# Performance work log

Measured on AMD Instinct MI355X. Metric: run time of the kernel, lower is better.

## Reference

```python
import jax, jax.numpy as jnp
import numpy as np

N_NODES = 50000
N_EDGES = 800000
N_FEAT = 256
HIDDEN = 64
N_CLASSES = 16
T_END = 3.0  # opt['time']; rk4 takes one step over [0, 3]


def spline_conv(x, src, dst, p, W, R, b, n):
    """SplineConv, dim=1, kernel_size=2, degree=1 open B-spline, aggr='mean'.
    x: [n, Cin]; src/dst: [E]; p: [E,1] pseudo-coords in [0,1];
    W: [2, Cin, Cout]; R: [Cin, Cout]; b: [Cout]."""
    xj = x[src]  # gather source node features [E, Cin]
    # basis weights for K=2, degree=1: (1-p) on kernel 0, p on kernel 1
    msg = ((1.0 - p) * xj) @ W[0] + (p * xj) @ W[1]  # [E, Cout]
    agg = jax.ops.segment_sum(msg, dst, num_segments=n)
    deg = jax.ops.segment_sum(jnp.ones((msg.shape[0], 1), msg.dtype), dst, num_segments=n)
    return agg / jnp.maximum(deg, 1.0) + x @ R + b


def setup_inputs() -> dict:
    key = jax.random.key(0)
    ks = jax.random.split(key, 20)
    x = jax.random.normal(ks[0], (N_NODES, N_FEAT), jnp.float32)
    edge_attr = jax.random.uniform(ks[1], (N_EDGES, 1), jnp.float32)
    src = jax.random.randint(ks[2], (N_EDGES,), 0, N_NODES)
    dst = jax.random.randint(ks[3], (N_EDGES,), 0, N_NODES)

    def w(k, shape, fan_in):
        s = 1.0 / np.sqrt(fan_in)
        return jax.random.uniform(k, shape, jnp.float32, -s, s)

    # conv1: num_features -> hidden
    W1 = w(ks[4], (2, N_FEAT, HIDDEN), N_FEAT)
    R1 = w(ks[5], (N_FEAT, HIDDEN), N_FEAT)
    b1 = jnp.zeros((HIDDEN,), jnp.float32)
    # ODE func: two stacked SplineConvs hidden -> hidden
    Wa = w(ks[6], (2, HIDDEN, HIDDEN), HIDDEN)
    Ra = w(ks[7], (HIDDEN, HIDDEN), HIDDEN)
    ba = jnp.zeros((HIDDEN,), jnp.float32)
    Wb = w(ks[8], (2, HIDDEN, HIDDEN), HIDDEN)
    Rb = w(ks[9], (HIDDEN, HIDDEN), HIDDEN)
    bb = jnp.zeros((HIDDEN,), jnp.float32)
    # conv2: hidden -> num_classes
    W2 = w(ks[10], (2, HIDDEN, N_CLASSES), HIDDEN)
    R2 = w(ks[11], (HIDDEN, N_CLASSES), HIDDEN)
    b2 = jnp.zeros((N_CLASSES,), jnp.float32)

    return dict(x=x, edge_attr=edge_attr, src=src, dst=dst,
                W1=W1, R1=R1, b1=b1, Wa=Wa, Ra=Ra, ba=ba,
                Wb=Wb, Rb=Rb, bb=bb, W2=W2, R2=R2, b2=b2)


def reference(x, edge_attr, src, dst, W1, R1, b1, Wa, Ra, ba, Wb, Rb, bb, W2, R2, b2):
    n = x.shape[0]
    p = edge_attr
    h = jnp.tanh(spline_conv(x, src, dst, p, W1, R1, b1, n))
    # dropout is identity in eval mode

    def f(y):  # GCNLayer: two stacked SplineConvs, no activation
        y = spline_conv(y, src, dst, p, Wa, Ra, ba, n)
        return spline_conv(y, src, dst, p, Wb, Rb, bb, n)

    # single RK4 step from t=0 to t=T_END (torchdiffeq fixed-grid rk4 on s_span=[0,3])
    k1 = f(h)
    k2 = f(h + 0.5 * T_END * k1)
    k3 = f(h + 0.5 * T_END * k2)
    k4 = f(h + T_END * k3)
    h = h + (T_END / 6.0) * (k1 + 2.0 * k2 + 2.0 * k3 + k4)

    out = jnp.tanh(spline_conv(h, src, dst, p, W2, R2, b2, n))
    return jax.nn.log_softmax(out, axis=1)
```

## Files before the change

### kernel.cpp

```cpp
#include <hip/hip_runtime.h>
#include <math.h>

static inline int ceil_div(int a, int b) { return (a + b - 1) / b; }


__global__ __launch_bounds__(256) void hist_kernel(const int* __restrict__ dst,
                                                   int* __restrict__ deg, int E) {
    int e = blockIdx.x * 256 + threadIdx.x;
    if (e < E) atomicAdd(&deg[dst[e]], 1);
}

__global__ __launch_bounds__(256) void scan_blocksum(const int* __restrict__ deg,
                                                     int* __restrict__ bsum, int n) {
    __shared__ int red[256];
    int t = threadIdx.x;
    int base = blockIdx.x * 2048 + t * 8;
    int s = 0;
    #pragma unroll
    for (int i = 0; i < 8; ++i) {
        int idx = base + i;
        if (idx < n) s += deg[idx];
    }
    red[t] = s;
    __syncthreads();
    #pragma unroll
    for (int off = 128; off >= 1; off >>= 1) {
        if (t < off) red[t] += red[t + off];
        __syncthreads();
    }
    if (t == 0) bsum[blockIdx.x] = red[0];
}

__global__ __launch_bounds__(256) void scan_tops(int* __restrict__ bsum, int nb) {
    __shared__ int sh[256];
    int t = threadIdx.x;
    int orig = (t < nb) ? bsum[t] : 0;
    sh[t] = orig;
    __syncthreads();
    for (int off = 1; off < 256; off <<= 1) {
        int add = (t >= off) ? sh[t - off] : 0;
        __syncthreads();
        sh[t] += add;
        __syncthreads();
    }
    if (t < nb) bsum[t] = sh[t] - orig;
}

__global__ __launch_bounds__(256) void scan_final(const int* __restrict__ deg,
                                                  const int* __restrict__ bsum,
                                                  int* __restrict__ rowp,
                                                  float* __restrict__ invd,
                                                  int n, int E) {
    __shared__ int sh[256];
    int t = threadIdx.x;
    int base = blockIdx.x * 2048 + t * 8;
    int loc[8];
    int s = 0;
    #pragma unroll
    for (int i = 0; i < 8; ++i) {
        int idx = base + i;
        int d = (idx < n) ? deg[idx] : 0;
        loc[i] = d;
        s += d;
    }
    sh[t] = s;
    __syncthreads();
    for (int off = 1; off < 256; off <<= 1) {
        int add = (t >= off) ? sh[t - off] : 0;
        __syncthreads();
        sh[t] += add;
        __syncthreads();
    }
    int run = bsum[blockIdx.x] + (sh[t] - s);
    #pragma unroll
    for (int i = 0; i < 8; ++i) {
        int idx = base + i;
        if (idx < n) {
            rowp[idx] = run;
            int d = loc[i];
            run += d;
            invd[idx] = 1.0f / (float)(d > 1 ? d : 1);
        }
    }
    if (blockIdx.x == 0 && t == 0) rowp[n] = E;
}

__global__ __launch_bounds__(256) void scatter_idx(const int* __restrict__ dst,
                                                   const int* __restrict__ rowp,
                                                   int* __restrict__ fill,
                                                   int* __restrict__ ei, int E) {
    int e = blockIdx.x * 256 + threadIdx.x;
    if (e >= E) return;
    int d = dst[e];
    int pos = rowp[d] + atomicAdd(&fill[d], 1);
    ei[pos] = e;
}

__global__ __launch_bounds__(256) void sort_fill(const int* __restrict__ rowp,
                                                 int* __restrict__ ei,
                                                 const int* __restrict__ src,
                                                 const float* __restrict__ p,
                                                 int* __restrict__ es,
                                                 float* __restrict__ ep, int n) {
    int node = blockIdx.x * 256 + threadIdx.x;
    if (node >= n) return;
    int b = rowp[node], e = rowp[node + 1];
    for (int i = b + 1; i < e; ++i) {
        int key = ei[i];
        int j = i - 1;
        while (j >= b && ei[j] > key) { ei[j + 1] = ei[j]; --j; }
        ei[j + 1] = key;
    }
    for (int i = b; i < e; ++i) {
        int id = ei[i];
        es[i] = src[id];
        ep[i] = p[id];
    }
}

__global__ __launch_bounds__(256) void pack_cat3(const float* __restrict__ W,
                                                 const float* __restrict__ R,
                                                 float* __restrict__ out, int K, int C) {
    int idx = blockIdx.x * 256 + threadIdx.x;
    int M = 3 * C;
    if (idx >= K * M) return;
    int k = idx / M, c = idx % M;
    float v;
    if (c < C)            v = W[k * C + c];
    else if (c < 2 * C)   v = W[K * C + k * C + (c - C)];
    else                  v = R[k * C + (c - 2 * C)];
    out[idx] = v;
}


__global__ __launch_bounds__(256) void edge_agg64_v4(const float* __restrict__ x,
                                                     const int* __restrict__ rowp,
                                                     const int* __restrict__ es,
                                                     const float* __restrict__ ep,
                                                     const float* __restrict__ invd,
                                                     float* __restrict__ agg, int n) {
    int gid = blockIdx.x * 256 + threadIdx.x;
    int node = gid >> 4;
    if (node >= n) return;
    int c4 = (gid & 15) << 2;
    int e = rowp[node], eend = rowp[node + 1];
    float sx = 0.f, sy = 0.f, sz = 0.f, sw = 0.f;
    float px = 0.f, py = 0.f, pz = 0.f, pw = 0.f;
    for (; e + 4 <= eend; e += 4) {
        int s0 = es[e], s1 = es[e + 1], s2 = es[e + 2], s3 = es[e + 3];
        float p0 = ep[e], p1 = ep[e + 1], p2 = ep[e + 2], p3 = ep[e + 3];
        float4 v0 = *reinterpret_cast<const float4*>(&x[(size_t)s0 * 64 + c4]);
        float4 v1 = *reinterpret_cast<const float4*>(&x[(size_t)s1 * 64 + c4]);
        float4 v2 = *reinterpret_cast<const float4*>(&x[(size_t)s2 * 64 + c4]);
        float4 v3 = *reinterpret_cast<const float4*>(&x[(size_t)s3 * 64 + c4]);
        sx += (v0.x + v1.x) + (v2.x + v3.x);
        sy += (v0.y + v1.y) + (v2.y + v3.y);
        sz += (v0.z + v1.z) + (v2.z + v3.z);
        sw += (v0.w + v1.w) + (v2.w + v3.w);
        px = fmaf(p0, v0.x, fmaf(p1, v1.x, fmaf(p2, v2.x, fmaf(p3, v3.x, px))));
        py = fmaf(p0, v0.y, fmaf(p1, v1.y, fmaf(p2, v2.y, fmaf(p3, v3.y, py))));
        pz = fmaf(p0, v0.z, fmaf(p1, v1.z, fmaf(p2, v2.z, fmaf(p3, v3.z, pz))));
        pw = fmaf(p0, v0.w, fmaf(p1, v1.w, fmaf(p2, v2.w, fmaf(p3, v3.w, pw))));
    }
    for (; e < eend; ++e) {
        int s = es[e];
        float pe = ep[e];
        float4 v = *reinterpret_cast<const float4*>(&x[(size_t)s * 64 + c4]);
        sx += v.x; sy += v.y; sz += v.z; sw += v.w;
        px = fmaf(pe, v.x, px); py = fmaf(pe, v.y, py);
        pz = fmaf(pe, v.z, pz); pw = fmaf(pe, v.w, pw);
    }
    float w = invd[node];
    float4 a0 = make_float4((sx - px) * w, (sy - py) * w, (sz - pz) * w, (sw - pw) * w);
    float4 a1 = make_float4(px * w, py * w, pz * w, pw * w);
    *reinterpret_cast<float4*>(&agg[(size_t)node * 128 + c4]) = a0;
    *reinterpret_cast<float4*>(&agg[(size_t)node * 128 + 64 + c4]) = a1;
}

__global__ __launch_bounds__(256) void edge_tf64_v4(const float* __restrict__ yz,
                                                    const int* __restrict__ rowp,
                                                    const int* __restrict__ es,
                                                    const float* __restrict__ ep,
                                                    const float* __restrict__ invd,
                                                    const float* __restrict__ base,
                                                    float* __restrict__ out, int n) {
    int gid = blockIdx.x * 256 + threadIdx.x;
    int node = gid >> 4;
    if (node >= n) return;
    int c4 = (gid & 15) << 2;
    int e = rowp[node], eend = rowp[node + 1];
    float ax = 0.f, ay = 0.f, az = 0.f, aw = 0.f;
    for (; e + 2 <= eend; e += 2) {
        int s0 = es[e], s1 = es[e + 1];
        float p0 = ep[e], p1 = ep[e + 1];
        float4 y0 = *reinterpret_cast<const float4*>(&yz[(size_t)s0 * 128 + c4]);
        float4 z0 = *reinterpret_cast<const float4*>(&yz[(size_t)s0 * 128 + 64 + c4]);
        float4 y1 = *reinterpret_cast<const float4*>(&yz[(size_t)s1 * 128 + c4]);
        float4 z1 = *reinterpret_cast<const float4*>(&yz[(size_t)s1 * 128 + 64 + c4]);
        ax += fmaf(p0, z0.x - y0.x, y0.x) + fmaf(p1, z1.x - y1.x, y1.x);
        ay += fmaf(p0, z0.y - y0.y, y0.y) + fmaf(p1, z1.y - y1.y, y1.y);
        az += fmaf(p0, z0.z - y0.z, y0.z) + fmaf(p1, z1.z - y1.z, y1.z);
        aw += fmaf(p0, z0.w - y0.w, y0.w) + fmaf(p1, z1.w - y1.w, y1.w);
    }
    for (; e < eend; ++e) {
        int s = es[e];
        float pe = ep[e];
        float4 y = *reinterpret_cast<const float4*>(&yz[(size_t)s * 128 + c4]);
        float4 z = *reinterpret_cast<const float4*>(&yz[(size_t)s * 128 + 64 + c4]);
        ax += fmaf(pe, z.x - y.x, y.x);
        ay += fmaf(pe, z.y - y.y, y.y);
        az += fmaf(pe, z.z - y.z, y.z);
        aw += fmaf(pe, z.w - y.w, y.w);
    }
    float w = invd[node];
    size_t idx = (size_t)node * 64 + c4;
    float4 b = *reinterpret_cast<const float4*>(&base[idx]);
    float4 o = make_float4(tanhf(fmaf(ax, w, b.x)), tanhf(fmaf(ay, w, b.y)),
                           tanhf(fmaf(az, w, b.z)), tanhf(fmaf(aw, w, b.w)));
    *reinterpret_cast<float4*>(&out[idx]) = o;
}

__global__ __launch_bounds__(256) void edge_tf16_lsm(const float* __restrict__ yz,
                                                     const int* __restrict__ rowp,
                                                     const int* __restrict__ es,
                                                     const float* __restrict__ ep,
                                                     const float* __restrict__ invd,
                                                     const float* __restrict__ base,
                                                     float* __restrict__ out, int n) {
    int gid = blockIdx.x * 256 + threadIdx.x;
    int node = gid >> 4;
    if (node >= n) return;
    int c = gid & 15;
    int e = rowp[node], eend = rowp[node + 1];
    float a = 0.f;
    for (; e + 4 <= eend; e += 4) {
        int s0 = es[e], s1 = es[e + 1], s2 = es[e + 2], s3 = es[e + 3];
        float p0 = ep[e], p1 = ep[e + 1], p2 = ep[e + 2], p3 = ep[e + 3];
        float y0 = yz[(size_t)s0 * 32 + c],      z0 = yz[(size_t)s0 * 32 + 16 + c];
        float y1 = yz[(size_t)s1 * 32 + c],      z1 = yz[(size_t)s1 * 32 + 16 + c];
        float y2 = yz[(size_t)s2 * 32 + c],      z2 = yz[(size_t)s2 * 32 + 16 + c];
        float y3 = yz[(size_t)s3 * 32 + c],      z3 = yz[(size_t)s3 * 32 + 16 + c];
        a += fmaf(p0, z0 - y0, y0);
        a += fmaf(p1, z1 - y1, y1);
        a += fmaf(p2, z2 - y2, y2);
        a += fmaf(p3, z3 - y3, y3);
    }
    for (; e < eend; ++e) {
        int s = es[e]; float pe = ep[e];
        float y = yz[(size_t)s * 32 + c], z = yz[(size_t)s * 32 + 16 + c];
        a += fmaf(pe, z - y, y);
    }
    float o = tanhf(a * invd[node] + base[(size_t)node * 16 + c]);
    float m = o;
    #pragma unroll
    for (int off = 8; off >= 1; off >>= 1) m = fmaxf(m, __shfl_xor(m, off, 16));
    float ex = expf(o - m);
    float s = ex;
    #pragma unroll
    for (int off = 8; off >= 1; off >>= 1) s += __shfl_xor(s, off, 16);
    out[(size_t)node * 16 + c] = (o - m) - logf(s);
}

__global__ __launch_bounds__(256) void gemm_tiled(
    const float* __restrict__ A0, int lda0, int K0,
    const float* __restrict__ A1, int lda1,
    const float* __restrict__ B,
    int n, int K, int M,
    float* __restrict__ out0, int w0, const float* __restrict__ bias0,
    float* __restrict__ out1, int w1, const float* __restrict__ bias1,
    int split, int mode,
    const float* __restrict__ hbuf, const float* __restrict__ acc_in,
    float* __restrict__ acc_out, float* __restrict__ t_out,
    float c1, float c2, float c3) {
    __shared__ __align__(16) float As[16][68];
    __shared__ __align__(16) float Bs[16][68];
    const int t = threadIdx.x;
    const int row0 = blockIdx.x * 64;
    const int col0 = blockIdx.y * 64;
    const int ty = t >> 4, tx = t & 15;
    const int lrow = t >> 2, lk = (t & 3) << 2;
    const int bkk = t >> 4, bcol = (t & 15) << 2;
    float acc[4][4];
    #pragma unroll
    for (int i = 0; i < 4; ++i)
        #pragma unroll
        for (int j = 0; j < 4; ++j) acc[i][j] = 0.f;

    for (int k0 = 0; k0 < K; k0 += 16) {
        float4 av = make_float4(0.f, 0.f, 0.f, 0.f);
        {
            int r = row0 + lrow;
            if (r < n) {
                int kk = k0 + lk;
                const float* src = (kk < K0)
                    ? (A0 + (size_t)r * lda0 + kk)
                    : (A1 + (size_t)r * lda1 + (kk - K0));
                av = *reinterpret_cast<const float4*>(src);
            }
        }
        float4 bv = make_float4(0.f, 0.f, 0.f, 0.f);
        {
            int c = col0 + bcol;
            int kk = k0 + bkk;
            if (c < M) bv = *reinterpret_cast<const float4*>(B + (size_t)kk * M + c);
        }
        As[lk + 0][lrow] = av.x; As[lk + 1][lrow] = av.y;
        As[lk + 2][lrow] = av.z; As[lk + 3][lrow] = av.w;
        *reinterpret_cast<float4*>(&Bs[bkk][bcol]) = bv;
        __syncthreads();
        #pragma unroll
        for (int kk = 0; kk < 16; ++kk) {
            float4 a4 = *reinterpret_cast<const float4*>(&As[kk][ty << 2]);
            float4 b4 = *reinterpret_cast<const float4*>(&Bs[kk][tx << 2]);
            float aa[4] = {a4.x, a4.y, a4.z, a4.w};
            float bb[4] = {b4.x, b4.y, b4.z, b4.w};
            #pragma unroll
            for (int i = 0; i < 4; ++i)
                #pragma unroll
                for (int j = 0; j < 4; ++j)
                    acc[i][j] = fmaf(aa[i], bb[j], acc[i][j]);
        }
        __syncthreads();
    }

    #pragma unroll
    for (int i = 0; i < 4; ++i) {
        int r = row0 + (ty << 2) + i;
        if (r >= n) continue;
        #pragma unroll
        for (int j = 0; j < 4; ++j) {
            int c = col0 + (tx << 2) + j;
            if (c >= M) continue;
            float v = acc[i][j];
            if (mode == 0) {
                if (c < split) {
                    if (bias0) v += bias0[c];
                    out0[(size_t)r * w0 + c] = v;
                } else {
                    int cc = c - split;
                    if (bias1) v += bias1[cc];
                    out1[(size_t)r * w1 + cc] = v;
                }
            } else {
                if (bias0) v += bias0[c];
                size_t idx = (size_t)r * 64 + c;
                float an = (acc_in ? acc_in[idx] : 0.f) + c3 * v;
                acc_out[idx] = an;
                t_out[idx] = hbuf[idx] + c1 * v + c2 * an;
            }
        }
    }
}


static void hidden_conv(hipStream_t stream, const float* in, float* big0,
                        const int* rowp, const int* es, const float* ep,
                        const float* invd, const float* Bc, const float* bias, int n,
                        int mode, float* out_plain,
                        const float* h, const float* acc_in, float* acc_out,
                        float* t_out, float c1, float c2, float c3) {
    edge_agg64_v4<<<ceil_div(n * 16, 256), 256, 0, stream>>>(in, rowp, es, ep, invd, big0, n);
    dim3 g(ceil_div(n, 64), 1);
    gemm_tiled<<<g, 256, 0, stream>>>(big0, 128, 128, in, 64, Bc, n, 192, 64,
                                      out_plain, 64, bias, nullptr, 0, nullptr, 64, mode,
                                      h, acc_in, acc_out, t_out, c1, c2, c3);
}

extern "C" void kernel_launch(void* const* d_in, const int* in_sizes, int n_in,
                              void* d_out, int out_size, void* d_ws, size_t ws_size,
                              hipStream_t stream) {
    const float* x  = (const float*)d_in[0];
    const float* pE = (const float*)d_in[1];
    const int*   sr = (const int*)d_in[2];
    const int*   ds = (const int*)d_in[3];
    const float* W1 = (const float*)d_in[4];
    const float* R1 = (const float*)d_in[5];
    const float* b1 = (const float*)d_in[6];
    const float* Wa = (const float*)d_in[7];
    const float* Ra = (const float*)d_in[8];
    const float* ba = (const float*)d_in[9];
    const float* Wb = (const float*)d_in[10];
    const float* Rb = (const float*)d_in[11];
    const float* bb = (const float*)d_in[12];
    const float* W2 = (const float*)d_in[13];
    const float* R2 = (const float*)d_in[14];
    const float* b2 = (const float*)d_in[15];
    const int n = in_sizes[0] / 256;
    const int E = in_sizes[2];
    float* out = (float*)d_out;

    char* w = (char*)d_ws;
    auto alloc = [&](size_t bytes) -> void* {
        void* ptr = (void*)w;
        w += (bytes + 255) & ~(size_t)255;
        return ptr;
    };
    int nscan = ceil_div(n, 2048);
    int*   deg  = (int*)alloc((size_t)n * 4);
    int*   fill = (int*)alloc((size_t)n * 4);
    int*   rowp = (int*)alloc((size_t)(n + 1) * 4);
    float* invd = (float*)alloc((size_t)n * 4);
    int*   bsum = (int*)alloc((size_t)256 * 4);
    int*   ei   = (int*)alloc((size_t)E * 4);
    int*   es   = (int*)alloc((size_t)E * 4);
    float* ep   = (float*)alloc((size_t)E * 4);
    float* Bc1  = (float*)alloc((size_t)256 * 192 * 4);
    float* Bca  = (float*)alloc((size_t)192 * 64 * 4);
    float* Bcb  = (float*)alloc((size_t)192 * 64 * 4);
    float* Bc2  = (float*)alloc((size_t)64 * 48 * 4);
    float* big0 = (float*)alloc((size_t)n * 128 * 4);
    float* big1 = (float*)alloc((size_t)n * 64 * 4);
    float* h    = (float*)alloc((size_t)n * 64 * 4);
    float* u    = (float*)alloc((size_t)n * 64 * 4);
    float* tb   = (float*)alloc((size_t)n * 64 * 4);
    float* acc  = (float*)alloc((size_t)n * 64 * 4);

    hipMemsetAsync(deg, 0, (size_t)n * 4, stream);
    hipMemsetAsync(fill, 0, (size_t)n * 4, stream);

    pack_cat3<<<ceil_div(256 * 192, 256), 256, 0, stream>>>(W1, R1, Bc1, 256, 64);
    pack_cat3<<<ceil_div(64 * 48, 256), 256, 0, stream>>>(W2, R2, Bc2, 64, 16);
    hipMemcpyAsync(Bca, Wa, (size_t)8192 * 4, hipMemcpyDeviceToDevice, stream);
    hipMemcpyAsync(Bca + 8192, Ra, (size_t)4096 * 4, hipMemcpyDeviceToDevice, stream);
    hipMemcpyAsync(Bcb, Wb, (size_t)8192 * 4, hipMemcpyDeviceToDevice, stream);
    hipMemcpyAsync(Bcb + 8192, Rb, (size_t)4096 * 4, hipMemcpyDeviceToDevice, stream);

    hist_kernel<<<ceil_div(E, 256), 256, 0, stream>>>(ds, deg, E);
    scan_blocksum<<<nscan, 256, 0, stream>>>(deg, bsum, n);
    scan_tops<<<1, 256, 0, stream>>>(bsum, nscan);
    scan_final<<<nscan, 256, 0, stream>>>(deg, bsum, rowp, invd, n, E);
    scatter_idx<<<ceil_div(E, 256), 256, 0, stream>>>(ds, rowp, fill, ei, E);
    sort_fill<<<ceil_div(n, 256), 256, 0, stream>>>(rowp, ei, sr, pE, es, ep, n);

    {
        dim3 g(ceil_div(n, 64), 3);
        gemm_tiled<<<g, 256, 0, stream>>>(x, 256, 256, nullptr, 0, Bc1, n, 256, 192,
                                          big0, 128, nullptr, big1, 64, b1, 128, 0,
                                          nullptr, nullptr, nullptr, nullptr, 0.f, 0.f, 0.f);
        edge_tf64_v4<<<ceil_div(n * 16, 256), 256, 0, stream>>>(big0, rowp, es, ep, invd,
                                                                big1, h, n);
    }

    hidden_conv(stream, h, big0, rowp, es, ep, invd, Bca, ba, n, 0, u,
                nullptr, nullptr, nullptr, nullptr, 0.f, 0.f, 0.f);
    hidden_conv(stream, u, big0, rowp, es, ep, invd, Bcb, bb, n, 1, nullptr,
                h, nullptr, acc, tb, 1.5f, 0.f, 1.f);
    hidden_conv(stream, tb, big0, rowp, es, ep, invd, Bca, ba, n, 0, u,
                nullptr, nullptr, nullptr, nullptr, 0.f, 0.f, 0.f);
    hidden_conv(stream, u, big0, rowp, es, ep, invd, Bcb, bb, n, 1, nullptr,
                h, acc, acc, tb, 1.5f, 0.f, 2.f);
    hidden_conv(stream, tb, big0, rowp, es, ep, invd, Bca, ba, n, 0, u,
                nullptr, nullptr, nullptr, nullptr, 0.f, 0.f, 0.f);
    hidden_conv(stream, u, big0, rowp, es, ep, invd, Bcb, bb, n, 1, nullptr,
                h, acc, acc, tb, 3.f, 0.f, 2.f);
    hidden_conv(stream, tb, big0, rowp, es, ep, invd, Bca, ba, n, 0, u,
                nullptr, nullptr, nullptr, nullptr, 0.f, 0.f, 0.f);
    hidden_conv(stream, u, big0, rowp, es, ep, invd, Bcb, bb, n, 1, nullptr,
                h, acc, acc, tb, 0.f, 0.5f, 1.f);

    {
        dim3 g(ceil_div(n, 64), 1);
        gemm_tiled<<<g, 256, 0, stream>>>(tb, 64, 64, nullptr, 0, Bc2, n, 64, 48,
                                          big0, 32, nullptr, big1, 16, b2, 32, 0,
                                          nullptr, nullptr, nullptr, nullptr, 0.f, 0.f, 0.f);
        edge_tf16_lsm<<<ceil_div(n * 16, 256), 256, 0, stream>>>(big0, rowp, es, ep, invd,
                                                                 big1, out, n);
    }
}
```

Baseline: 951.7 us.

## Fuse edge aggregation with GEMM in hidden convs and merge setup kernels

Each hidden SplineConv now does the CSR edge aggregation for a 64-node tile straight into shared memory and runs the 192x64 GEMM with its epilogue in the same kernel. This drops the big0 intermediate round-trip and one launch per conv. The conv1 GEMM becomes a dedicated kernel where each thread computes all 192 output columns, so x is read once instead of three times. Weight packing and memsets are merged into single kernels. In exchange, the fused kernel uses about 53KB of shared memory, which can lower occupancy during the latency-bound gather phase.

```diff
diff --git a/kernel.cpp b/kernel.cpp
--- a/kernel.cpp
+++ b/kernel.cpp
@@ -3,6 +3,12 @@
 
 static inline int ceil_div(int a, int b) { return (a + b - 1) / b; }
 
+
+__global__ __launch_bounds__(256) void zero2(int* __restrict__ a, int* __restrict__ b,
+                                             int n) {
+    int i = blockIdx.x * 256 + threadIdx.x;
+    if (i < n) { a[i] = 0; b[i] = 0; }
+}
 
 __global__ __launch_bounds__(256) void hist_kernel(const int* __restrict__ dst,
                                                    int* __restrict__ deg, int E) {
@@ -118,64 +124,225 @@
     }
 }
 
-__global__ __launch_bounds__(256) void pack_cat3(const float* __restrict__ W,
-                                                 const float* __restrict__ R,
-                                                 float* __restrict__ out, int K, int C) {
+__global__ __launch_bounds__(256) void pack_all(
+    const float* __restrict__ W1, const float* __restrict__ R1,
+    const float* __restrict__ Wa, const float* __restrict__ Ra,
+    const float* __restrict__ Wb, const float* __restrict__ Rb,
+    const float* __restrict__ W2, const float* __restrict__ R2,
+    float* __restrict__ Bc1, float* __restrict__ Bca,
+    float* __restrict__ Bcb, float* __restrict__ Bc2) {
     int idx = blockIdx.x * 256 + threadIdx.x;
-    int M = 3 * C;
-    if (idx >= K * M) return;
-    int k = idx / M, c = idx % M;
-    float v;
-    if (c < C)            v = W[k * C + c];
-    else if (c < 2 * C)   v = W[K * C + k * C + (c - C)];
-    else                  v = R[k * C + (c - 2 * C)];
-    out[idx] = v;
-}
-
-
-__global__ __launch_bounds__(256) void edge_agg64_v4(const float* __restrict__ x,
-                                                     const int* __restrict__ rowp,
-                                                     const int* __restrict__ es,
-                                                     const float* __restrict__ ep,
-                                                     const float* __restrict__ invd,
-                                                     float* __restrict__ agg, int n) {
-    int gid = blockIdx.x * 256 + threadIdx.x;
-    int node = gid >> 4;
-    if (node >= n) return;
-    int c4 = (gid & 15) << 2;
-    int e = rowp[node], eend = rowp[node + 1];
-    float sx = 0.f, sy = 0.f, sz = 0.f, sw = 0.f;
-    float px = 0.f, py = 0.f, pz = 0.f, pw = 0.f;
-    for (; e + 4 <= eend; e += 4) {
-        int s0 = es[e], s1 = es[e + 1], s2 = es[e + 2], s3 = es[e + 3];
-        float p0 = ep[e], p1 = ep[e + 1], p2 = ep[e + 2], p3 = ep[e + 3];
-        float4 v0 = *reinterpret_cast<const float4*>(&x[(size_t)s0 * 64 + c4]);
-        float4 v1 = *reinterpret_cast<const float4*>(&x[(size_t)s1 * 64 + c4]);
-        float4 v2 = *reinterpret_cast<const float4*>(&x[(size_t)s2 * 64 + c4]);
-        float4 v3 = *reinterpret_cast<const float4*>(&x[(size_t)s3 * 64 + c4]);
-        sx += (v0.x + v1.x) + (v2.x + v3.x);
-        sy += (v0.y + v1.y) + (v2.y + v3.y);
-        sz += (v0.z + v1.z) + (v2.z + v3.z);
-        sw += (v0.w + v1.w) + (v2.w + v3.w);
-        px = fmaf(p0, v0.x, fmaf(p1, v1.x, fmaf(p2, v2.x, fmaf(p3, v3.x, px))));
-        py = fmaf(p0, v0.y, fmaf(p1, v1.y, fmaf(p2, v2.y, fmaf(p3, v3.y, py))));
-        pz = fmaf(p0, v0.z, fmaf(p1, v1.z, fmaf(p2, v2.z, fmaf(p3, v3.z, pz))));
-        pw = fmaf(p0, v0.w, fmaf(p1, v1.w, fmaf(p2, v2.w, fmaf(p3, v3.w, pw))));
-    }
-    for (; e < eend; ++e) {
-        int s = es[e];
-        float pe = ep[e];
-        float4 v = *reinterpret_cast<const float4*>(&x[(size_t)s * 64 + c4]);
-        sx += v.x; sy += v.y; sz += v.z; sw += v.w;
-        px = fmaf(pe, v.x, px); py = fmaf(pe, v.y, py);
-        pz = fmaf(pe, v.z, pz); pw = fmaf(pe, v.w, pw);
-    }
-    float w = invd[node];
-    float4 a0 = make_float4((sx - px) * w, (sy - py) * w, (sz - pz) * w, (sw - pw) * w);
-    float4 a1 = make_float4(px * w, py * w, pz * w, pw * w);
-    *reinterpret_cast<float4*>(&agg[(size_t)node * 128 + c4]) = a0;
-    *reinterpret_cast<float4*>(&agg[(size_t)node * 128 + 64 + c4]) = a1;
-}
+    const int S1 = 256 * 192, S2 = 192 * 64, S4 = 64 * 48;
+    if (idx < S1) {
+        int k = idx / 192, c = idx % 192;
+        float v;
+        if (c < 64)       v = W1[k * 64 + c];
+        else if (c < 128) v = W1[256 * 64 + k * 64 + (c - 64)];
+        else              v = R1[k * 64 + (c - 128)];
+        Bc1[idx] = v;
+        return;
+    }
+    idx -= S1;
+    if (idx < S2) { Bca[idx] = (idx < 8192) ? Wa[idx] : Ra[idx - 8192]; return; }
+    idx -= S2;
+    if (idx < S2) { Bcb[idx] = (idx < 8192) ? Wb[idx] : Rb[idx - 8192]; return; }
+    idx -= S2;
+    if (idx < S4) {
+        int k = idx / 48, c = idx % 48;
+        float v;
+        if (c < 16)      v = W2[k * 16 + c];
+        else if (c < 32) v = W2[64 * 16 + k * 16 + (c - 16)];
+        else             v = R2[k * 16 + (c - 32)];
+        Bc2[idx] = v;
+    }
+}
+
+__global__ __launch_bounds__(256) void conv1_gemm(const float* __restrict__ x,
+                                                  const float* __restrict__ B,
+                                                  int n, float* __restrict__ yz,
+                                                  float* __restrict__ base,
+                                                  const float* __restrict__ b1) {
+    __shared__ __align__(16) float As[16][68];
+    __shared__ __align__(16) float Bs[16][200];
+    const int t = threadIdx.x;
+    const int row0 = blockIdx.x * 64;
+    const int ty = t >> 4, tx = t & 15;
+    const int lrow = t >> 2, lk = (t & 3) << 2;
+    const int bkk = t >> 4, bcol = (t & 15) << 2;
+    float acc[4][12];
+    #pragma unroll
+    for (int i = 0; i < 4; ++i)
+        #pragma unroll
+        for (int j = 0; j < 12; ++j) acc[i][j] = 0.f;
+
+    for (int k0 = 0; k0 < 256; k0 += 16) {
+        float4 av = make_float4(0.f, 0.f, 0.f, 0.f);
+        int r = row0 + lrow;
+        if (r < n) av = *reinterpret_cast<const float4*>(&x[(size_t)r * 256 + k0 + lk]);
+        As[lk + 0][lrow] = av.x; As[lk + 1][lrow] = av.y;
+        As[lk + 2][lrow] = av.z; As[lk + 3][lrow] = av.w;
+        const float* bp = &B[(size_t)(k0 + bkk) * 192 + bcol];
+        *reinterpret_cast<float4*>(&Bs[bkk][bcol])       = *reinterpret_cast<const float4*>(bp);
+        *reinterpret_cast<float4*>(&Bs[bkk][bcol + 64])  = *reinterpret_cast<const float4*>(bp + 64);
+        *reinterpret_cast<float4*>(&Bs[bkk][bcol + 128]) = *reinterpret_cast<const float4*>(bp + 128);
+        __syncthreads();
+        #pragma unroll
+        for (int kk = 0; kk < 16; ++kk) {
+            float4 a4 = *reinterpret_cast<const float4*>(&As[kk][ty << 2]);
+            float4 b0 = *reinterpret_cast<const float4*>(&Bs[kk][tx << 2]);
+            float4 b1v = *reinterpret_cast<const float4*>(&Bs[kk][(tx << 2) + 64]);
+            float4 b2v = *reinterpret_cast<const float4*>(&Bs[kk][(tx << 2) + 128]);
+            float aa[4] = {a4.x, a4.y, a4.z, a4.w};
+            float bb[12] = {b0.x, b0.y, b0.z, b0.w, b1v.x, b1v.y, b1v.z, b1v.w,
+                            b2v.x, b2v.y, b2v.z, b2v.w};
+            #pragma unroll
+            for (int i = 0; i < 4; ++i)
+                #pragma unroll
+                for (int j = 0; j < 12; ++j)
+                    acc[i][j] = fmaf(aa[i], bb[j], acc[i][j]);
+        }
+        __syncthreads();
+    }
+
+    float4 bb4 = *reinterpret_cast<const float4*>(&b1[tx << 2]);
+    #pragma unroll
+    for (int i = 0; i < 4; ++i) {
+        int r = row0 + (ty << 2) + i;
+        if (r >= n) continue;
+        float4 q0 = make_float4(acc[i][0], acc[i][1], acc[i][2], acc[i][3]);
+        float4 q1 = make_float4(acc[i][4], acc[i][5], acc[i][6], acc[i][7]);
+        float4 q2 = make_float4(acc[i][8] + bb4.x, acc[i][9] + bb4.y,
+                                acc[i][10] + bb4.z, acc[i][11] + bb4.w);
+        *reinterpret_cast<float4*>(&yz[(size_t)r * 128 + (tx << 2)]) = q0;
+        *reinterpret_cast<float4*>(&yz[(size_t)r * 128 + 64 + (tx << 2)]) = q1;
+        *reinterpret_cast<float4*>(&base[(size_t)r * 64 + (tx << 2)]) = q2;
+    }
+}
+
+__global__ __launch_bounds__(256) void hidden_fused(
+    const float* __restrict__ in, const int* __restrict__ rowp,
+    const int* __restrict__ es, const float* __restrict__ ep,
+    const float* __restrict__ invd, const float* __restrict__ B,
+    const float* __restrict__ bias, int n, int mode,
+    float* __restrict__ u_out,
+    const float* __restrict__ hbuf, const float* __restrict__ acc_in,
+    float* __restrict__ acc_out, float* __restrict__ t_out,
+    float c1, float c2, float c3) {
+    __shared__ __align__(16) float As[192][68];
+    __shared__ __align__(16) float Bs[16][68];
+    const int t = threadIdx.x;
+    const int row0 = blockIdx.x * 64;
+    const int c4 = (t & 15) << 2;
+    const int ng = t >> 4;
+
+    for (int sub = 0; sub < 4; ++sub) {
+        int nl = (sub << 4) + ng;
+        int node = row0 + nl;
+        if (node < n) {
+            int e = rowp[node], eend = rowp[node + 1];
+            float sx = 0.f, sy = 0.f, sz = 0.f, sw = 0.f;
+            float px = 0.f, py = 0.f, pz = 0.f, pw = 0.f;
+            for (; e + 4 <= eend; e += 4) {
+                int a = es[e], b = es[e + 1], c = es[e + 2], d = es[e + 3];
+                float pa = ep[e], pb = ep[e + 1], pc = ep[e + 2], pd = ep[e + 3];
+                float4 va = *reinterpret_cast<const float4*>(&in[(size_t)a * 64 + c4]);
+                float4 vb = *reinterpret_cast<const float4*>(&in[(size_t)b * 64 + c4]);
+                float4 vc = *reinterpret_cast<const float4*>(&in[(size_t)c * 64 + c4]);
+                float4 vd = *reinterpret_cast<const float4*>(&in[(size_t)d * 64 + c4]);
+                sx += (va.x + vb.x) + (vc.x + vd.x);
+                sy += (va.y + vb.y) + (vc.y + vd.y);
+                sz += (va.z + vb.z) + (vc.z + vd.z);
+                sw += (va.w + vb.w) + (vc.w + vd.w);
+                px = fmaf(pa, va.x, fmaf(pb, vb.x, fmaf(pc, vc.x, fmaf(pd, vd.x, px))));
+                py = fmaf(pa, va.y, fmaf(pb, vb.y, fmaf(pc, vc.y, fmaf(pd, vd.y, py))));
+                pz = fmaf(pa, va.z, fmaf(pb, vb.z, fmaf(pc, vc.z, fmaf(pd, vd.z, pz))));
+                pw = fmaf(pa, va.w, fmaf(pb, vb.w, fmaf(pc, vc.w, fmaf(pd, vd.w, pw))));
+            }
+            for (; e < eend; ++e) {
+                int s = es[e];
+                float pe = ep[e];
+                float4 v = *reinterpret_cast<const float4*>(&in[(size_t)s * 64 + c4]);
+                sx += v.x; sy += v.y; sz += v.z; sw += v.w;
+                px = fmaf(pe, v.x, px); py = fmaf(pe, v.y, py);
+                pz = fmaf(pe, v.z, pz); pw = fmaf(pe, v.w, pw);
+            }
+            float w = invd[node];
+            float4 r4 = *reinterpret_cast<const float4*>(&in[(size_t)node * 64 + c4]);
+            As[c4 + 0][nl] = (sx - px) * w;
+            As[c4 + 1][nl] = (sy - py) * w;
+            As[c4 + 2][nl] = (sz - pz) * w;
+            As[c4 + 3][nl] = (sw - pw) * w;
+            As[64 + c4 + 0][nl] = px * w;
+            As[64 + c4 + 1][nl] = py * w;
+            As[64 + c4 + 2][nl] = pz * w;
+            As[64 + c4 + 3][nl] = pw * w;
+            As[128 + c4 + 0][nl] = r4.x;
+            As[128 + c4 + 1][nl] = r4.y;
+            As[128 + c4 + 2][nl] = r4.z;
+            As[128 + c4 + 3][nl] = r4.w;
+        } else {
+            #pragma unroll
+            for (int i = 0; i < 4; ++i) {
+                As[c4 + i][nl] = 0.f;
+                As[64 + c4 + i][nl] = 0.f;
+                As[128 + c4 + i][nl] = 0.f;
+            }
+        }
+    }
+    __syncthreads();
+
+    const int ty = t >> 4, tx = t & 15;
+    float acc[4][4];
+    #pragma unroll
+    for (int i = 0; i < 4; ++i)
+        #pragma unroll
+        for (int j = 0; j < 4; ++j) acc[i][j] = 0.f;
+
+    for (int s = 0; s < 12; ++s) {
+        *reinterpret_cast<float4*>(&Bs[t >> 4][(t & 15) << 2]) =
+            *reinterpret_cast<const float4*>(&B[(size_t)((s << 4) + (t >> 4)) * 64 + ((t & 15) << 2)]);
+        __syncthreads();
+        #pragma unroll
+        for (int kk = 0; kk < 16; ++kk) {
+            float4 a4 = *reinterpret_cast<const float4*>(&As[(s << 4) + kk][ty << 2]);
+            float4 b4 = *reinterpret_cast<const float4*>(&Bs[kk][tx << 2]);
+            float aa[4] = {a4.x, a4.y, a4.z, a4.w};
+            float bb[4] = {b4.x, b4.y, b4.z, b4.w};
+            #pragma unroll
+            for (int i = 0; i < 4; ++i)
+                #pragma unroll
+                for (int j = 0; j < 4; ++j)
+                    acc[i][j] = fmaf(aa[i], bb[j], acc[i][j]);
+        }
+        __syncthreads();
+    }
+
+    float4 bv = *reinterpret_cast<const float4*>(&bias[tx << 2]);
+    #pragma unroll
+    for (int i = 0; i < 4; ++i) {
+        int r = row0 + (ty << 2) + i;
+        if (r >= n) continue;
+        size_t idx = (size_t)r * 64 + (tx << 2);
+        float4 v = make_float4(acc[i][0] + bv.x, acc[i][1] + bv.y,
+                               acc[i][2] + bv.z, acc[i][3] + bv.w);
+        if (mode == 0) {
+            *reinterpret_cast<float4*>(&u_out[idx]) = v;
+        } else {
+            float4 ai = make_float4(0.f, 0.f, 0.f, 0.f);
+            if (acc_in) ai = *reinterpret_cast<const float4*>(&acc_in[idx]);
+            float4 an = make_float4(ai.x + c3 * v.x, ai.y + c3 * v.y,
+                                    ai.z + c3 * v.z, ai.w + c3 * v.w);
+            *reinterpret_cast<float4*>(&acc_out[idx]) = an;
+            float4 hb = *reinterpret_cast<const float4*>(&hbuf[idx]);
+            float4 to = make_float4(hb.x + c1 * v.x + c2 * an.x,
+                                    hb.y + c1 * v.y + c2 * an.y,
+                                    hb.z + c1 * v.z + c2 * an.z,
+                                    hb.w + c1 * v.w + c2 * an.w);
+            *reinterpret_cast<float4*>(&t_out[idx]) = to;
+        }
+    }
+}
+
 
 __global__ __launch_bounds__(256) void edge_tf64_v4(const float* __restrict__ yz,
                                                     const int* __restrict__ rowp,
@@ -332,39 +499,18 @@
             int c = col0 + (tx << 2) + j;
             if (c >= M) continue;
             float v = acc[i][j];
-            if (mode == 0) {
-                if (c < split) {
-                    if (bias0) v += bias0[c];
-                    out0[(size_t)r * w0 + c] = v;
-                } else {
-                    int cc = c - split;
-                    if (bias1) v += bias1[cc];
-                    out1[(size_t)r * w1 + cc] = v;
-                }
+            if (c < split) {
+                if (bias0) v += bias0[c];
+                out0[(size_t)r * w0 + c] = v;
             } else {
-                if (bias0) v += bias0[c];
-                size_t idx = (size_t)r * 64 + c;
-                float an = (acc_in ? acc_in[idx] : 0.f) + c3 * v;
-                acc_out[idx] = an;
-                t_out[idx] = hbuf[idx] + c1 * v + c2 * an;
+                int cc = c - split;
+                if (bias1) v += bias1[cc];
+                out1[(size_t)r * w1 + cc] = v;
             }
         }
     }
 }
 
-
-static void hidden_conv(hipStream_t stream, const float* in, float* big0,
-                        const int* rowp, const int* es, const float* ep,
-                        const float* invd, const float* Bc, const float* bias, int n,
-                        int mode, float* out_plain,
-                        const float* h, const float* acc_in, float* acc_out,
-                        float* t_out, float c1, float c2, float c3) {
-    edge_agg64_v4<<<ceil_div(n * 16, 256), 256, 0, stream>>>(in, rowp, es, ep, invd, big0, n);
-    dim3 g(ceil_div(n, 64), 1);
-    gemm_tiled<<<g, 256, 0, stream>>>(big0, 128, 128, in, 64, Bc, n, 192, 64,
-                                      out_plain, 64, bias, nullptr, 0, nullptr, 64, mode,
-                                      h, acc_in, acc_out, t_out, c1, c2, c3);
-}
 
 extern "C" void kernel_launch(void* const* d_in, const int* in_sizes, int n_in,
                               void* d_out, int out_size, void* d_ws, size_t ws_size,
@@ -415,16 +561,11 @@
     float* tb   = (float*)alloc((size_t)n * 64 * 4);
     float* acc  = (float*)alloc((size_t)n * 64 * 4);
 
-    hipMemsetAsync(deg, 0, (size_t)n * 4, stream);
-    hipMemsetAsync(fill, 0, (size_t)n * 4, stream);
-
-    pack_cat3<<<ceil_div(256 * 192, 256), 256, 0, stream>>>(W1, R1, Bc1, 256, 64);
-    pack_cat3<<<ceil_div(64 * 48, 256), 256, 0, stream>>>(W2, R2, Bc2, 64, 16);
-    hipMemcpyAsync(Bca, Wa, (size_t)8192 * 4, hipMemcpyDeviceToDevice, stream);
-    hipMemcpyAsync(Bca + 8192, Ra, (size_t)4096 * 4, hipMemcpyDeviceToDevice, stream);
-    hipMemcpyAsync(Bcb, Wb, (size_t)8192 * 4, hipMemcpyDeviceToDevice, stream);
-    hipMemcpyAsync(Bcb + 8192, Rb, (size_t)4096 * 4, hipMemcpyDeviceToDevice, stream);
-
+    const int PACK_TOTAL = 256 * 192 + 2 * 192 * 64 + 64 * 48;
+
+    zero2<<<ceil_div(n, 256), 256, 0, stream>>>(deg, fill, n);
+    pack_all<<<ceil_div(PACK_TOTAL, 256), 256, 0, stream>>>(W1, R1, Wa, Ra, Wb, Rb,
+                                                            W2, R2, Bc1, Bca, Bcb, Bc2);
     hist_kernel<<<ceil_div(E, 256), 256, 0, stream>>>(ds, deg, E);
     scan_blocksum<<<nscan, 256, 0, stream>>>(deg, bsum, n);
     scan_tops<<<1, 256, 0, stream>>>(bsum, nscan);
@@ -432,34 +573,31 @@
     scatter_idx<<<ceil_div(E, 256), 256, 0, stream>>>(ds, rowp, fill, ei, E);
     sort_fill<<<ceil_div(n, 256), 256, 0, stream>>>(rowp, ei, sr, pE, es, ep, n);
 
+    const int gb = ceil_div(n, 64);
+
+    conv1_gemm<<<gb, 256, 0, stream>>>(x, Bc1, n, big0, big1, b1);
+    edge_tf64_v4<<<ceil_div(n * 16, 256), 256, 0, stream>>>(big0, rowp, es, ep, invd,
+                                                            big1, h, n);
+
+    hidden_fused<<<gb, 256, 0, stream>>>(h, rowp, es, ep, invd, Bca, ba, n, 0, u,
+                                         nullptr, nullptr, nullptr, nullptr, 0.f, 0.f, 0.f);
+    hidden_fused<<<gb, 256, 0, stream>>>(u, rowp, es, ep, invd, Bcb, bb, n, 1, nullptr,
+                                         h, nullptr, acc, tb, 1.5f, 0.f, 1.f);
+    hidden_fused<<<gb, 256, 0, stream>>>(tb, rowp, es, ep, invd, Bca, ba, n, 0, u,
+                                         nullptr, nullptr, nullptr, nullptr, 0.f, 0.f, 0.f);
+    hidden_fused<<<gb, 256, 0, stream>>>(u, rowp, es, ep, invd, Bcb, bb, n, 1, nullptr,
+                                         h, acc, acc, tb, 1.5f, 0.f, 2.f);
+    hidden_fused<<<gb, 256, 0, stream>>>(tb, rowp, es, ep, invd, Bca, ba, n, 0, u,
+                                         nullptr, nullptr, nullptr, nullptr, 0.f, 0.f, 0.f);
+    hidden_fused<<<gb, 256, 0, stream>>>(u, rowp, es, ep, invd, Bcb, bb, n, 1, nullptr,
+                                         h, acc, acc, tb, 3.f, 0.f, 2.f);
+    hidden_fused<<<gb, 256, 0, stream>>>(tb, rowp, es, ep, invd, Bca, ba, n, 0, u,
+                                         nullptr, nullptr, nullptr, nullptr, 0.f, 0.f, 0.f);
+    hidden_fused<<<gb, 256, 0, stream>>>(u, rowp, es, ep, invd, Bcb, bb, n, 1, nullptr,
+                                         h, acc, acc, tb, 0.f, 0.5f, 1.f);
+
     {
-        dim3 g(ceil_div(n, 64), 3);
-        gemm_tiled<<<g, 256, 0, stream>>>(x, 256, 256, nullptr, 0, Bc1, n, 256, 192,
-                                          big0, 128, nullptr, big1, 64, b1, 128, 0,
-                                          nullptr, nullptr, nullptr, nullptr, 0.f, 0.f, 0.f);
-        edge_tf64_v4<<<ceil_div(n * 16, 256), 256, 0, stream>>>(big0, rowp, es, ep, invd,
-                                                                big1, h, n);
-    }
-
-    hidden_conv(stream, h, big0, rowp, es, ep, invd, Bca, ba, n, 0, u,
-                nullptr, nullptr, nullptr, nullptr, 0.f, 0.f, 0.f);
-    hidden_conv(stream, u, big0, rowp, es, ep, invd, Bcb, bb, n, 1, nullptr,
-                h, nullptr, acc, tb, 1.5f, 0.f, 1.f);
-    hidden_conv(stream, tb, big0, rowp, es, ep, invd, Bca, ba, n, 0, u,
-                nullptr, nullptr, nullptr, nullptr, 0.f, 0.f, 0.f);
-    hidden_conv(stream, u, big0, rowp, es, ep, invd, Bcb, bb, n, 1, nullptr,
-                h, acc, acc, tb, 1.5f, 0.f, 2.f);
-    hidden_conv(stream, tb, big0, rowp, es, ep, invd, Bca, ba, n, 0, u,
-                nullptr, nullptr, nullptr, nullptr, 0.f, 0.f, 0.f);
-    hidden_conv(stream, u, big0, rowp, es, ep, invd, Bcb, bb, n, 1, nullptr,
-                h, acc, acc, tb, 3.f, 0.f, 2.f);
-    hidden_conv(stream, tb, big0, rowp, es, ep, invd, Bca, ba, n, 0, u,
-                nullptr, nullptr, nullptr, nullptr, 0.f, 0.f, 0.f);
-    hidden_conv(stream, u, big0, rowp, es, ep, invd, Bcb, bb, n, 1, nullptr,
-                h, acc, acc, tb, 0.f, 0.5f, 1.f);
-
-    {
-        dim3 g(ceil_div(n, 64), 1);
+        dim3 g(gb, 1);
         gemm_tiled<<<g, 256, 0, stream>>>(tb, 64, 64, nullptr, 0, Bc2, n, 64, 48,
                                           big0, 32, nullptr, big1, 16, b2, 32, 0,
                                           nullptr, nullptr, nullptr, nullptr, 0.f, 0.f, 0.f);
```

New measurement: 996.4 us. 4.7% more time.
